# Kernel optimization log

Hardware: AMD Instinct MI355X
Metric: run time of the kernel (lower is better)

The kernel has to match this reference:

```python
import jax, jax.numpy as jnp
import numpy as np

B, N, FEAT, BB, LD = 512, 50, 300, 300, 2048
D1 = BB + FEAT        # 600 = s_with_bb dim
D2 = 2 * D1           # 1200 = combined dim


def _fc(x, w, b):
    # ReLUWithWeightNormFC: weight-norm is a reparametrization of a plain
    # linear, so math-equivalently ReLU(x @ W^T + b).
    return jax.nn.relu(x @ w.T + b)


def setup_inputs() -> dict:
    key = jax.random.key(0)
    ks = jax.random.split(key, 32)

    def p(k, shape):
        return jax.random.normal(k, shape, dtype=jnp.float32) * 0.02

    inp = {
        "l": jax.random.normal(ks[0], (B, LD), dtype=jnp.float32),
        "s": jax.random.normal(ks[1], (B, N, FEAT), dtype=jnp.float32),
        "ps": jax.random.uniform(ks[2], (B, N, 4), dtype=jnp.float32),
        "mask_s": jax.random.randint(ks[3], (B,), 0, 50, dtype=jnp.int32),
        "bb_w": p(ks[4], (BB, 10)),       "bb_b": p(ks[5], (BB,)),
        "fa1_w": p(ks[6], (D1, D1)),      "fa1_b": p(ks[7], (D1,)),
        "fa2_w": p(ks[8], (D1, D1)),      "fa2_b": p(ks[9], (D1,)),
        "fa3_w": p(ks[10], (D2, D2)),     "fa3_b": p(ks[11], (D2,)),
        "fa4_w": p(ks[12], (D2, D2)),     "fa4_b": p(ks[13], (D2,)),
        "fa5_w": p(ks[14], (D2, D2)),     "fa5_b": p(ks[15], (D2,)),
        "lp1_w": p(ks[16], (D2, LD)),     "lp1_b": p(ks[17], (D2,)),
        "lp2_w": p(ks[18], (D2, LD)),     "lp2_b": p(ks[19], (D2,)),
        "out_w": p(ks[20], (FEAT, D2)),   "out_b": p(ks[21], (FEAT,)),
    }
    return inp


def reference(l, s, ps, mask_s,
              bb_w, bb_b, fa1_w, fa1_b, fa2_w, fa2_b, fa3_w, fa3_b,
              fa4_w, fa4_b, fa5_w, fa5_b, lp1_w, lp1_b, lp2_w, lp2_b,
              out_w, out_b):
    # ---- bb_process ----
    size = ps[..., 2:] - ps[..., :2]                       # [B,N,2]
    centre = ps[..., :2] + 0.5 * size                      # [B,N,2]
    area = (size[..., 0] * size[..., 1])[..., None]        # [B,N,1]
    shape = (size[..., 0] / (size[..., 1] + 1e-14))[..., None]
    bb_in = jnp.concatenate([ps, size, centre, area, shape], axis=-1)  # [B,N,10]
    bb = _fc(bb_in, bb_w, bb_b)                            # [B,N,BB]

    s_bb = jnp.concatenate([s, bb], axis=-1)               # [B,N,D1]

    # ---- masked adjacency bias (order of assignments preserved) ----
    i = jnp.arange(N)
    mx = jnp.maximum(i[None, :], i[:, None])               # [N,N]
    m1 = mx[None, :, :] < mask_s[:, None, None]            # [B,N,N]
    m2 = i[None, :, None] >= mask_s[:, None, None]         # row index >= mask_s
    inf_tmp = jnp.where(m1 | m2, 0.0, -jnp.inf)
    inf_tmp = jnp.where(jnp.eye(N, dtype=bool)[None], -jnp.inf, inf_tmp)
    inf_tmp = inf_tmp.at[:, 0, 0].set(
        jnp.where(mask_s == 1, 0.0, inf_tmp[:, 0, 0]))

    # l projections are identical across the 50 nodes -> compute once, broadcast
    lp1 = _fc(l, lp1_w, lp1_b)[:, None, :]                 # [B,1,D2]
    lp2 = _fc(l, lp2_w, lp2_b)[:, None, :]                 # [B,1,D2]

    # ---- one GNN iteration (it=1) ----
    combined = jnp.concatenate(
        [s_bb, _fc(s_bb, fa1_w, fa1_b) * _fc(s_bb, fa2_w, fa2_b)], axis=-1)  # [B,N,D2]
    l_masked_source = _fc(combined, fa3_w, fa3_b) * lp1    # [B,N,D2]
    adj = jnp.einsum('bnd,bmd->bnm', _fc(combined, fa4_w, fa4_b),
                     l_masked_source)                      # [B,N,N]
    adj = jax.nn.softmax(adj + inf_tmp, axis=2)
    prepared = _fc(combined, fa5_w, fa5_b) * lp2           # [B,N,D2]
    messages = _fc(jnp.einsum('bnm,bmd->bnd', adj, prepared), out_w, out_b)
    s_out = jnp.concatenate([s, messages], axis=-1)        # [B,N,2*FEAT]

    output_mask = (i[None, :] < mask_s[:, None])[:, :, None]  # [B,N,1]
    return s_out * output_mask.astype(s_out.dtype), adj
```

## Files before the change

kernel.cpp:

```cpp
#include <hip/hip_runtime.h>
#include <stdint.h>

typedef unsigned short u16;
typedef unsigned int u32;
typedef __attribute__((ext_vector_type(8))) __bf16 bf16x8;
typedef __attribute__((ext_vector_type(4))) float f32x4;

#define DEVINL static __device__ __forceinline__

DEVINL u16 f2bf(float x) {
  u32 u = __float_as_uint(x);
  return (u16)((u + (((u >> 16) & 1u) + 0x7fffu)) >> 16);
}
DEVINL float bf2f(u16 h) { return __uint_as_float(((u32)h) << 16); }

DEVINL void async16(const void* g, void* l) {
  void* g2 = const_cast<void*>(g);
  __builtin_amdgcn_global_load_lds((__attribute__((address_space(1))) void*)g2,
                                   (__attribute__((address_space(3))) void*)l,
                                   16, 0, 0);
}

DEVINL void swz_xy(int& bx, int& by) {
  const int gx = (int)gridDim.x;
  const int nwg = gx * (int)gridDim.y;
  const int bid = (int)blockIdx.y * gx + (int)blockIdx.x;
  const int q = nwg >> 3, r = nwg & 7, x = bid & 7, t = bid >> 3;
  const int s = (x < r ? x * (q + 1) : r * (q + 1) + (x - r) * q) + t;
  bx = s % gx;
  by = s / gx;
}


__global__ void k_pack_w(const float* src, int n, int k, u16* hi, u16* lo,
                         int KP, long total, int gap) {
  long i = (long)blockIdx.x * 256 + threadIdx.x;
  if (i >= total) return;
  int r = (int)(i / KP);
  int c = (int)(i - (long)r * KP);
  int sc = c;
  bool ok = (r < n);
  if (gap) {
    if (c >= 600 && c < 640) ok = false;
    else if (c >= 640) sc = c - 40;
  }
  if (sc >= k) ok = false;
  float x = ok ? src[(size_t)r * k + sc] : 0.f;
  u16 h = f2bf(x);
  hi[i] = h;
  if (lo) lo[i] = f2bf(x - bf2f(h));
}

__global__ void k_pack_bias(const float* src, int n, float* dst, int NP) {
  int i = blockIdx.x * 256 + threadIdx.x;
  if (i < NP) dst[i] = (i < n) ? src[i] : 0.f;
}

__global__ void k_bb(const float* s_c, const float* ps_c, const float* bb_w,
                     const float* bb_b, u16* Chi, u16* Clo) {
  int rn = blockIdx.x;
  const float* p = ps_c + (size_t)rn * 4;
  float p0 = p[0], p1 = p[1], p2 = p[2], p3 = p[3];
  float sz0 = p2 - p0, sz1 = p3 - p1;
  float bin[10];
  bin[0] = p0; bin[1] = p1; bin[2] = p2; bin[3] = p3;
  bin[4] = sz0; bin[5] = sz1;
  bin[6] = p0 + 0.5f * sz0; bin[7] = p1 + 0.5f * sz1;
  bin[8] = sz0 * sz1; bin[9] = sz0 / (sz1 + 1e-14f);
  for (int c = threadIdx.x; c < 640; c += 256) {
    float x = 0.f;
    if (c < 300) {
      x = s_c[(size_t)rn * 300 + c];
    } else if (c < 600) {
      int j = c - 300;
      float a = bb_b[j];
      const float* wr = bb_w + j * 10;
#pragma unroll
      for (int kk = 0; kk < 10; ++kk) a += bin[kk] * wr[kk];
      x = fmaxf(a, 0.f);
    }
    u16 h = f2bf(x);
    Chi[(size_t)rn * 1280 + c] = h;
    Clo[(size_t)rn * 1280 + c] = f2bf(x - bf2f(h));
  }
}


DEVINL void gemm_fused3(const u16* Ahp, const u16* Alp, const u16* Bhp,
                        const u16* Blp, int lda, int ldw, int ksteps,
                        u16* S, f32x4 (&acc)[4][4]) {
  const int tid = threadIdx.x;
  const int lane = tid & 63;
  const int wv = tid >> 6;
  const int wr = (wv >> 1) * 64;
  const int wc = (wv & 1) * 64;
  const int mrow = lane & 15;
  const int q = lane >> 4;

  const int c0 = tid, c1 = tid + 256;
  const int p0 = ((c0 & 3) ^ ((c0 >> 3) & 3)) * 8;
  const int p1 = ((c1 & 3) ^ ((c1 >> 3) & 3)) * 8;
  const long ao0 = (long)(c0 >> 2) * lda + p0;
  const long ao1 = (long)(c1 >> 2) * lda + p1;
  const long bo0 = (long)(c0 >> 2) * ldw + p0;
  const long bo1 = (long)(c1 >> 2) * ldw + p1;

  int aoffs[4], boffs[4];
#pragma unroll
  for (int k = 0; k < 4; ++k) {
    const int ra = wr + mrow + 16 * k;
    const int rb = wc + mrow + 16 * k;
    aoffs[k] = ra * 32 + ((q ^ ((ra >> 1) & 3)) << 3);
    boffs[k] = rb * 32 + ((q ^ ((rb >> 1) & 3)) << 3);
  }

  auto issue = [&](int sl, int t) {
    const long ta = (long)t * 32;
    u16* d = S + sl * 16384;
    async16(Ahp + ta + ao0, d + c0 * 8);
    async16(Ahp + ta + ao1, d + c1 * 8);
    async16(Alp + ta + ao0, d + 4096 + c0 * 8);
    async16(Alp + ta + ao1, d + 4096 + c1 * 8);
    async16(Bhp + ta + bo0, d + 8192 + c0 * 8);
    async16(Bhp + ta + bo1, d + 8192 + c1 * 8);
    async16(Blp + ta + bo0, d + 12288 + c0 * 8);
    async16(Blp + ta + bo1, d + 12288 + c1 * 8);
  };

  issue(0, 0);
  for (int i = 0; i < ksteps; ++i) {
    asm volatile("s_waitcnt vmcnt(0)" ::: "memory");
    __builtin_amdgcn_sched_barrier(0);
    __builtin_amdgcn_s_barrier();
    __builtin_amdgcn_sched_barrier(0);
    if (i + 1 < ksteps) issue((i + 1) & 1, i + 1);
    const u16* Sb = S + (i & 1) * 16384;
    bf16x8 ah[4], al[4], bh[4], bl[4];
#pragma unroll
    for (int k = 0; k < 4; ++k) {
      ah[k] = *(const bf16x8*)(Sb + aoffs[k]);
      al[k] = *(const bf16x8*)(Sb + 4096 + aoffs[k]);
      bh[k] = *(const bf16x8*)(Sb + 8192 + boffs[k]);
      bl[k] = *(const bf16x8*)(Sb + 12288 + boffs[k]);
    }
#pragma unroll
    for (int mi = 0; mi < 4; ++mi)
#pragma unroll
      for (int nj = 0; nj < 4; ++nj)
        acc[mi][nj] = __builtin_amdgcn_mfma_f32_16x16x32_bf16(
            ah[mi], bh[nj], acc[mi][nj], 0, 0, 0);
#pragma unroll
    for (int mi = 0; mi < 4; ++mi)
#pragma unroll
      for (int nj = 0; nj < 4; ++nj)
        acc[mi][nj] = __builtin_amdgcn_mfma_f32_16x16x32_bf16(
            al[mi], bh[nj], acc[mi][nj], 0, 0, 0);
#pragma unroll
    for (int mi = 0; mi < 4; ++mi)
#pragma unroll
      for (int nj = 0; nj < 4; ++nj)
        acc[mi][nj] = __builtin_amdgcn_mfma_f32_16x16x32_bf16(
            ah[mi], bl[nj], acc[mi][nj], 0, 0, 0);
  }
}

DEVINL void gemm_core1(const u16* Ab, const u16* Bb, int lda, int ldw,
                       int ksteps, u16* As, u16* Bs, f32x4 (&acc)[4][4]) {
  const int tid = threadIdx.x;
  const int lane = tid & 63;
  const int wv = tid >> 6;
  const int wr = (wv >> 1) * 64;
  const int wc = (wv & 1) * 64;
  const int mrow = lane & 15;
  const int q = lane >> 4;

  const int c0 = tid, c1 = tid + 256;
  const int p0 = ((c0 & 3) ^ ((c0 >> 3) & 3)) * 8;
  const int p1 = ((c1 & 3) ^ ((c1 >> 3) & 3)) * 8;
  const long ao0 = (long)(c0 >> 2) * lda + p0;
  const long ao1 = (long)(c1 >> 2) * lda + p1;
  const long bo0 = (long)(c0 >> 2) * ldw + p0;
  const long bo1 = (long)(c1 >> 2) * ldw + p1;

  int aoffs[4], boffs[4];
#pragma unroll
  for (int k = 0; k < 4; ++k) {
    const int ra = wr + mrow + 16 * k;
    const int rb = wc + mrow + 16 * k;
    aoffs[k] = ra * 32 + ((q ^ ((ra >> 1) & 3)) << 3);
    boffs[k] = rb * 32 + ((q ^ ((rb >> 1) & 3)) << 3);
  }

  auto issue = [&](int sl, int t) {
    const long ta = (long)t * 32;
    u16* dA = As + sl * 4096;
    u16* dB = Bs + sl * 4096;
    async16(Ab + ta + ao0, dA + c0 * 8);
    async16(Ab + ta + ao1, dA + c1 * 8);
    async16(Bb + ta + bo0, dB + c0 * 8);
    async16(Bb + ta + bo1, dB + c1 * 8);
  };

  issue(0, 0);
  if (ksteps > 1) issue(1, 1);
  if (ksteps > 2) issue(2, 2);
  for (int i = 0; i < ksteps; ++i) {
    if (i + 2 < ksteps)      asm volatile("s_waitcnt vmcnt(8)" ::: "memory");
    else if (i + 1 < ksteps) asm volatile("s_waitcnt vmcnt(4)" ::: "memory");
    else                     asm volatile("s_waitcnt vmcnt(0)" ::: "memory");
    __builtin_amdgcn_sched_barrier(0);
    __builtin_amdgcn_s_barrier();
    __builtin_amdgcn_sched_barrier(0);
    if (i + 3 < ksteps) issue((i + 3) & 3, i + 3);
    const u16* Sa = As + (i & 3) * 4096;
    const u16* Sb = Bs + (i & 3) * 4096;
    bf16x8 af[4], bv[4];
#pragma unroll
    for (int k = 0; k < 4; ++k) af[k] = *(const bf16x8*)(Sa + aoffs[k]);
#pragma unroll
    for (int k = 0; k < 4; ++k) bv[k] = *(const bf16x8*)(Sb + boffs[k]);
#pragma unroll
    for (int mi = 0; mi < 4; ++mi)
#pragma unroll
      for (int nj = 0; nj < 4; ++nj)
        acc[mi][nj] = __builtin_amdgcn_mfma_f32_16x16x32_bf16(
            af[mi], bv[nj], acc[mi][nj], 0, 0, 0);
  }
}

DEVINL void gemm_core2(const u16* const Aph[3], const u16* const B1ph[3],
                       const u16* const B2ph[3], int lda, int ldw, int ksteps,
                       u16* As, u16* B1s, u16* B2s, f32x4 (&a1)[4][4],
                       f32x4 (&a2)[4][4]) {
  const int tid = threadIdx.x;
  const int lane = tid & 63;
  const int wv = tid >> 6;
  const int wr = (wv >> 1) * 64;
  const int wc = (wv & 1) * 64;
  const int mrow = lane & 15;
  const int q = lane >> 4;

  const int c0 = tid, c1 = tid + 256;
  const int p0 = ((c0 & 3) ^ ((c0 >> 3) & 3)) * 8;
  const int p1 = ((c1 & 3) ^ ((c1 >> 3) & 3)) * 8;
  const long ao0 = (long)(c0 >> 2) * lda + p0;
  const long ao1 = (long)(c1 >> 2) * lda + p1;
  const long bo0 = (long)(c0 >> 2) * ldw + p0;
  const long bo1 = (long)(c1 >> 2) * ldw + p1;

  int aoffs[4], boffs[4];
#pragma unroll
  for (int k = 0; k < 4; ++k) {
    const int ra = wr + mrow + 16 * k;
    const int rb = wc + mrow + 16 * k;
    aoffs[k] = ra * 32 + ((q ^ ((ra >> 1) & 3)) << 3);
    boffs[k] = rb * 32 + ((q ^ ((rb >> 1) & 3)) << 3);
  }

  const u16* Aa1 = Aph[1]; const u16* Ba1 = B1ph[1]; const u16* Ca1 = B2ph[1];
  const u16* Aa2 = Aph[2]; const u16* Ba2 = B1ph[2]; const u16* Ca2 = B2ph[2];
  const u16* An = Aph[0];  const u16* Bn = B1ph[0];  const u16* Cn = B2ph[0];
  int tn = 0, pn = 0;
  const int total = 3 * ksteps;

  auto issue = [&](int sl) {
    const u16* ga = An + (long)tn * 32;
    const u16* g1 = Bn + (long)tn * 32;
    const u16* g2 = Cn + (long)tn * 32;
    u16* dA = As + sl * 4096;
    u16* d1 = B1s + sl * 4096;
    u16* d2 = B2s + sl * 4096;
    async16(ga + ao0, dA + c0 * 8);
    async16(ga + ao1, dA + c1 * 8);
    async16(g1 + bo0, d1 + c0 * 8);
    async16(g1 + bo1, d1 + c1 * 8);
    async16(g2 + bo0, d2 + c0 * 8);
    async16(g2 + bo1, d2 + c1 * 8);
    if (++tn == ksteps) {
      tn = 0; ++pn;
      if (pn == 1) { An = Aa1; Bn = Ba1; Cn = Ca1; }
      else if (pn == 2) { An = Aa2; Bn = Ba2; Cn = Ca2; }
    }
  };

  issue(0);
  issue(1);
  int slot = 0;
  for (int i = 0; i < total; ++i) {
    if (i + 1 < total) asm volatile("s_waitcnt vmcnt(6)" ::: "memory");
    else               asm volatile("s_waitcnt vmcnt(0)" ::: "memory");
    __builtin_amdgcn_sched_barrier(0);
    __builtin_amdgcn_s_barrier();
    __builtin_amdgcn_sched_barrier(0);
    if (i + 2 < total) {
      int s2 = slot + 2; if (s2 >= 3) s2 -= 3;
      issue(s2);
    }
    const u16* Sa = As + slot * 4096;
    const u16* S1 = B1s + slot * 4096;
    const u16* S2 = B2s + slot * 4096;
    bf16x8 af[4], b1v[4], b2v[4];
#pragma unroll
    for (int k = 0; k < 4; ++k) af[k] = *(const bf16x8*)(Sa + aoffs[k]);
#pragma unroll
    for (int k = 0; k < 4; ++k) b1v[k] = *(const bf16x8*)(S1 + boffs[k]);
#pragma unroll
    for (int k = 0; k < 4; ++k) b2v[k] = *(const bf16x8*)(S2 + boffs[k]);
#pragma unroll
    for (int mi = 0; mi < 4; ++mi)
#pragma unroll
      for (int nj = 0; nj < 4; ++nj)
        a1[mi][nj] = __builtin_amdgcn_mfma_f32_16x16x32_bf16(
            af[mi], b1v[nj], a1[mi][nj], 0, 0, 0);
#pragma unroll
    for (int mi = 0; mi < 4; ++mi)
#pragma unroll
      for (int nj = 0; nj < 4; ++nj)
        a2[mi][nj] = __builtin_amdgcn_mfma_f32_16x16x32_bf16(
            af[mi], b2v[nj], a2[mi][nj], 0, 0, 0);
    if (++slot == 3) slot = 0;
  }
}

#define GEMM_EPI_IDX                                                    \
  const int lane = threadIdx.x & 63, wv = threadIdx.x >> 6;             \
  const int wr = (wv >> 1) * 64, wc = (wv & 1) * 64;                    \
  const int mcol = lane & 15, q = lane >> 4;                            \
  const int gm0 = by * 128, gn0 = bx * 128;

__global__ __launch_bounds__(256) void k_gemm_fa12(const u16* Ah, const u16* Al,
    const u16* W1h, const u16* W1l, const u16* W2h, const u16* W2l,
    const float* bias, u16* Chi, u16* Clo) {
  __shared__ __align__(16) u16 As[12288], B1s[12288], B2s[12288];
  int bx, by; swz_xy(bx, by);
  const size_t arow = (size_t)by * 128 * 1280;
  const size_t wrow = (size_t)bx * 128 * 640;
  const u16* Aph[3]  = {Ah + arow, Al + arow, Ah + arow};
  const u16* B1ph[3] = {W1h + wrow, W1h + wrow, W1l + wrow};
  const u16* B2ph[3] = {W2h + wrow, W2h + wrow, W2l + wrow};
  f32x4 a1[4][4] = {}, a2[4][4] = {};
  gemm_core2(Aph, B1ph, B2ph, 1280, 640, 20, As, B1s, B2s, a1, a2);
  GEMM_EPI_IDX
#pragma unroll
  for (int mi = 0; mi < 4; ++mi)
#pragma unroll
    for (int r = 0; r < 4; ++r) {
      int grow = gm0 + wr + mi * 16 + q * 4 + r;
#pragma unroll
      for (int ni = 0; ni < 4; ++ni) {
        int gcol = gn0 + wc + ni * 16 + mcol;
        float v1 = fmaxf(a1[mi][ni][r] + bias[gcol], 0.f);
        float v2 = fmaxf(a2[mi][ni][r] + bias[640 + gcol], 0.f);
        float y = v1 * v2;
        u16 h = f2bf(y);
        Chi[(size_t)grow * 1280 + 640 + gcol] = h;
        Clo[(size_t)grow * 1280 + 640 + gcol] = f2bf(y - bf2f(h));
      }
    }
}

__global__ __launch_bounds__(256) void k_gemm_lp(const u16* Ah, const u16* Al,
    const u16* Wh, const u16* Wl, const float* bias, float* outp) {
  __shared__ __align__(16) u16 S[32768];
  int bx, by; swz_xy(bx, by);
  const size_t arow = (size_t)by * 128 * 2048;
  const size_t wrow = (size_t)bx * 128 * 2048;
  f32x4 acc[4][4] = {};
  gemm_fused3(Ah + arow, Al + arow, Wh + wrow, Wl + wrow, 2048, 2048, 64, S,
              acc);
  GEMM_EPI_IDX
#pragma unroll
  for (int mi = 0; mi < 4; ++mi)
#pragma unroll
    for (int r = 0; r < 4; ++r) {
      int grow = gm0 + wr + mi * 16 + q * 4 + r;
#pragma unroll
      for (int ni = 0; ni < 4; ++ni) {
        int gcol = gn0 + wc + ni * 16 + mcol;
        outp[(size_t)grow * 2560 + gcol] = fmaxf(acc[mi][ni][r] + bias[gcol], 0.f);
      }
    }
}

__global__ __launch_bounds__(256) void k_gemm_fa345(const u16* Ah, const u16* Al,
    const u16* Wh, const u16* Wl, const u16* W5h, const float* b34,
    const float* b5, const float* lp_o, u16* fa3h, u16* fa3l, u16* fa4h,
    u16* fa4l, u16* fa5o, int r0) {
  __shared__ __align__(16) u16 S[32768];
  int bx, by; swz_xy(bx, by);
  const size_t arow = (size_t)by * 128 * 1280;
  const int gn0 = bx * 128;
  f32x4 acc[4][4] = {};
  if (gn0 < 2560) {
    const size_t wrow = (size_t)gn0 * 1280;
    gemm_fused3(Ah + arow, Al + arow, Wh + wrow, Wl + wrow, 1280, 1280, 40, S,
                acc);
  } else {
    const size_t wrow = (size_t)(gn0 - 2560) * 1280;
    gemm_core1(Ah + arow, W5h + wrow, 1280, 1280, 40, S, S + 16384, acc);
  }
  const int lane = threadIdx.x & 63, wv = threadIdx.x >> 6;
  const int wr = (wv >> 1) * 64, wc = (wv & 1) * 64;
  const int mcol = lane & 15, q = lane >> 4;
  const int gm0 = by * 128;
  if (gn0 < 2560) {
    const int seg = (gn0 >= 1280);
    u16* dsth = seg ? fa4h : fa3h;
    u16* dstl = seg ? fa4l : fa3l;
#pragma unroll
    for (int mi = 0; mi < 4; ++mi)
#pragma unroll
      for (int r = 0; r < 4; ++r) {
        int grow = gm0 + wr + mi * 16 + q * 4 + r;
        int b = (r0 + grow) / 50;
        const float* lpb = lp_o + (size_t)b * 2560;
#pragma unroll
        for (int ni = 0; ni < 4; ++ni) {
          int gcol = gn0 + wc + ni * 16 + mcol;
          int c = seg ? gcol - 1280 : gcol;
          float v = fmaxf(acc[mi][ni][r] + b34[gcol], 0.f);
          if (!seg) v *= lpb[c];
          if (c < 1216) {
            u16 h = f2bf(v);
            dsth[(size_t)grow * 1216 + c] = h;
            dstl[(size_t)grow * 1216 + c] = f2bf(v - bf2f(h));
          }
        }
      }
  } else {
#pragma unroll
    for (int mi = 0; mi < 4; ++mi)
#pragma unroll
      for (int r = 0; r < 4; ++r) {
        int grow = gm0 + wr + mi * 16 + q * 4 + r;
        int b = (r0 + grow) / 50;
        const float* lpb = lp_o + (size_t)b * 2560 + 1280;
#pragma unroll
        for (int ni = 0; ni < 4; ++ni) {
          int gcol = (gn0 - 2560) + wc + ni * 16 + mcol;
          float v = fmaxf(acc[mi][ni][r] + b5[gcol], 0.f) * lpb[gcol];
          if (gcol < 1216) fa5o[(size_t)grow * 1216 + gcol] = f2bf(v);
        }
      }
  }
}

__global__ __launch_bounds__(256) void k_gemm_out(const u16* A, const u16* Wh,
    const float* bias, const int* mask_s, float* outp, int r0) {
  __shared__ __align__(16) u16 S[32768];
  int bx, by; swz_xy(bx, by);
  const size_t arow = (size_t)by * 128 * 1216;
  const size_t wrow = (size_t)bx * 128 * 1216;
  f32x4 acc[4][4] = {};
  gemm_core1(A + arow, Wh + wrow, 1216, 1216, 38, S, S + 16384, acc);
  GEMM_EPI_IDX
#pragma unroll
  for (int mi = 0; mi < 4; ++mi)
#pragma unroll
    for (int r = 0; r < 4; ++r) {
      int grow = r0 + gm0 + wr + mi * 16 + q * 4 + r;
      int b = grow / 50;
      int n = grow - b * 50;
      float keep = (n < mask_s[b]) ? 1.f : 0.f;
#pragma unroll
      for (int ni = 0; ni < 4; ++ni) {
        int gcol = gn0 + wc + ni * 16 + mcol;
        float v = fmaxf(acc[mi][ni][r] + bias[gcol], 0.f) * keep;
        if (gcol < 300) outp[(size_t)grow * 600 + 300 + gcol] = v;
      }
    }
}

__global__ __launch_bounds__(256) void k_attn(const u16* fa3h, const u16* fa3l,
    const u16* fa4h, const u16* fa4l, const u16* fa5o, const int* mask_s,
    float* adj_out, u16* msg, int b0) {
  __shared__ __align__(16) u16 stg[4096];
  __shared__ float Ssc[64 * 64];
  const int bl = blockIdx.x;
  const int bg = b0 + bl;
  const int tid = threadIdx.x, lane = tid & 63, wv = tid >> 6;
  const int mrow = lane & 15, q = lane >> 4;
  const size_t base = (size_t)bl * 50 * 1216;

  {
    const int srow = tid >> 2;
    const int srcRow = srow < 50 ? srow : 49;
    const size_t gsoff = base + (size_t)srcRow * 1216 + (tid & 3) * 8;
    u16* lA = stg + tid * 8;
    u16* lB = stg + 2048 + tid * 8;
    f32x4 acc[4] = {};
    for (int p = 0; p < 3; ++p) {
      const u16* Ap = (p == 1) ? fa4l : fa4h;
      const u16* Bp = (p == 2) ? fa3l : fa3h;
      for (int t = 0; t < 38; ++t) {
        __syncthreads();
        async16(Ap + gsoff + t * 32, lA);
        async16(Bp + gsoff + t * 32, lB);
        __syncthreads();
        bf16x8 af = *(const bf16x8*)(stg + (wv * 16 + mrow) * 32 + q * 8);
#pragma unroll
        for (int ni = 0; ni < 4; ++ni) {
          bf16x8 bv = *(const bf16x8*)(stg + 2048 + (ni * 16 + mrow) * 32 + q * 8);
          acc[ni] =
              __builtin_amdgcn_mfma_f32_16x16x32_bf16(af, bv, acc[ni], 0, 0, 0);
        }
      }
    }
#pragma unroll
    for (int ni = 0; ni < 4; ++ni)
#pragma unroll
      for (int r = 0; r < 4; ++r)
        Ssc[(wv * 16 + q * 4 + r) * 64 + ni * 16 + mrow] = acc[ni][r];
  }
  __syncthreads();

  {
    const int mk = mask_s[bg];
    for (int n = wv; n < 50; n += 4) {
      int mm = lane;
      float v = -__builtin_inff();
      if (mm < 50) {
        int mx2 = n > mm ? n : mm;
        bool valid = (mx2 < mk) || (n >= mk);
        if (mm == n) valid = false;
        if (n == 0 && mm == 0 && mk == 1) valid = true;
        if (valid) v = Ssc[n * 64 + mm];
      }
      float mx = v;
      for (int o = 32; o > 0; o >>= 1) mx = fmaxf(mx, __shfl_down(mx, o));
      mx = __shfl(mx, 0);
      float e = __expf(v - mx);
      float sm = e;
      for (int o = 32; o > 0; o >>= 1) sm += __shfl_down(sm, o);
      sm = __shfl(sm, 0);
      float pv = e / sm;
      if (mm < 50) {
        adj_out[((size_t)bg * 50 + n) * 50 + mm] = pv;
        Ssc[n * 64 + mm] = pv;
      } else {
        Ssc[n * 64 + mm] = 0.f;
      }
    }
  }
  __syncthreads();

  {
    const int c0 = tid, c1 = tid + 256;
    const int m0 = c0 >> 3, d0 = (c0 & 7) * 8;
    const int m1 = c1 >> 3, d1 = (c1 & 7) * 8;
    const size_t g0 = base + (size_t)(m0 < 50 ? m0 : 49) * 1216 + d0;
    const size_t g1 = base + (size_t)(m1 < 50 ? m1 : 49) * 1216 + d1;
    for (int dt = 0; dt < 19; ++dt) {
      __syncthreads();
      async16(fa5o + g0 + dt * 64, stg + c0 * 8);
      async16(fa5o + g1 + dt * 64, stg + c1 * 8);
      __syncthreads();
      f32x4 a3[4] = {};
#pragma unroll
      for (int ks = 0; ks < 2; ++ks) {
        bf16x8 af;
#pragma unroll
        for (int j = 0; j < 8; ++j)
          af[j] = (__bf16)Ssc[(wv * 16 + mrow) * 64 + ks * 32 + q * 8 + j];
#pragma unroll
        for (int ni = 0; ni < 4; ++ni) {
          bf16x8 bv;
#pragma unroll
          for (int j = 0; j < 8; ++j)
            bv[j] = *(const __bf16*)(stg + (ks * 32 + q * 8 + j) * 64 + ni * 16 + mrow);
          a3[ni] = __builtin_amdgcn_mfma_f32_16x16x32_bf16(af, bv, a3[ni], 0, 0, 0);
        }
      }
#pragma unroll
      for (int ni = 0; ni < 4; ++ni)
#pragma unroll
        for (int r = 0; r < 4; ++r) {
          int n = wv * 16 + q * 4 + r;
          if (n < 50)
            msg[((size_t)bl * 50 + n) * 1216 + dt * 64 + ni * 16 + mrow] =
                f2bf(a3[ni][r]);
        }
    }
  }
}

__global__ void k_write_s(const float* s, const int* mask_s, float* outp) {
  long i = (long)blockIdx.x * 256 + threadIdx.x;
  if (i >= 7680000L) return;
  int rn = (int)(i / 300);
  int c = (int)(i - (long)rn * 300);
  int b = rn / 50;
  int n = rn - b * 50;
  outp[(size_t)rn * 600 + c] = (n < mask_s[b]) ? s[i] : 0.f;
}

extern "C" void kernel_launch(void* const* d_in, const int* in_sizes, int n_in,
                              void* d_out_, int out_size, void* d_ws,
                              size_t ws_size, hipStream_t stream) {
  (void)in_sizes; (void)n_in; (void)out_size;
  const float* l_in = (const float*)d_in[0];
  const float* s_in = (const float*)d_in[1];
  const float* ps   = (const float*)d_in[2];
  const int*   msk  = (const int*)d_in[3];
  const float* bbw  = (const float*)d_in[4];
  const float* bbb  = (const float*)d_in[5];
  const float* fa1w = (const float*)d_in[6];
  const float* fa1b = (const float*)d_in[7];
  const float* fa2w = (const float*)d_in[8];
  const float* fa2b = (const float*)d_in[9];
  const float* fa3w = (const float*)d_in[10];
  const float* fa3b = (const float*)d_in[11];
  const float* fa4w = (const float*)d_in[12];
  const float* fa4b = (const float*)d_in[13];
  const float* fa5w = (const float*)d_in[14];
  const float* fa5b = (const float*)d_in[15];
  const float* lp1w = (const float*)d_in[16];
  const float* lp1b = (const float*)d_in[17];
  const float* lp2w = (const float*)d_in[18];
  const float* lp2b = (const float*)d_in[19];
  const float* outw = (const float*)d_in[20];
  const float* outb = (const float*)d_in[21];
  float* outp = (float*)d_out_;

  char* wsb = (char*)d_ws;
  size_t off = 0;
  auto alloc = [&](size_t bytes) -> char* {
    char* p = wsb + off;
    off = (off + bytes + 255) & ~(size_t)255;
    return p;
  };
  u16*   l_hi   = (u16*)alloc(512ull * 2048 * 2);
  u16*   l_lo   = (u16*)alloc(512ull * 2048 * 2);
  u16*   Wout   = (u16*)alloc(384ull * 1216 * 2);
  float* b_fa12 = (float*)alloc(1280 * 4);
  float* b_fa34 = (float*)alloc(2560 * 4);
  float* b_fa5  = (float*)alloc(1280 * 4);
  float* b_lp   = (float*)alloc(2560 * 4);
  float* b_out  = (float*)alloc(384 * 4);
  float* lp_o   = (float*)alloc(512ull * 2560 * 4);
  u16*   slab   = (u16*)alloc(10485760ull * 2);
  u16* Wlph   = slab;
  u16* Wlpl   = slab + 5242880;
  u16* Wfa1h  = slab;
  u16* Wfa1l  = slab + 409600;
  u16* Wfa2h  = slab + 819200;
  u16* Wfa2l  = slab + 1228800;
  u16* Wfa34h = slab + 1638400;
  u16* Wfa34l = slab + 4915200;
  u16* Wfa5h  = slab + 8192000;

  size_t ws_eff = ws_size ? ws_size : (size_t)512 * 1024 * 1024;
  long RN = 3200;
  const long opts[4] = {25600, 12800, 6400, 3200};
  for (int i = 0; i < 4; ++i) {
    size_t need = off + (size_t)17280 * opts[i] + 8 * 256;
    if (need <= ws_eff) { RN = opts[i]; break; }
  }
  u16*  Chi  = (u16*)alloc((size_t)RN * 1280 * 2);
  u16*  Clo  = (u16*)alloc((size_t)RN * 1280 * 2);
  u16*  fa5o = (u16*)alloc((size_t)RN * 1216 * 2);
  u16*  fa3h = (u16*)alloc((size_t)RN * 1216 * 2);
  u16*  fa3l = (u16*)alloc((size_t)RN * 1216 * 2);
  u16*  fa4h = (u16*)alloc((size_t)RN * 1216 * 2);
  u16*  fa4l = (u16*)alloc((size_t)RN * 1216 * 2);
  u16*  msg  = Chi;
  float* adj_o = outp + 15360000;

  dim3 T(256);
  k_pack_bias<<<dim3(3), T, 0, stream>>>(fa1b, 600, b_fa12, 640);
  k_pack_bias<<<dim3(3), T, 0, stream>>>(fa2b, 600, b_fa12 + 640, 640);
  k_pack_bias<<<dim3(5), T, 0, stream>>>(fa3b, 1200, b_fa34, 1280);
  k_pack_bias<<<dim3(5), T, 0, stream>>>(fa4b, 1200, b_fa34 + 1280, 1280);
  k_pack_bias<<<dim3(5), T, 0, stream>>>(fa5b, 1200, b_fa5, 1280);
  k_pack_bias<<<dim3(5), T, 0, stream>>>(lp1b, 1200, b_lp, 1280);
  k_pack_bias<<<dim3(5), T, 0, stream>>>(lp2b, 1200, b_lp + 1280, 1280);
  k_pack_bias<<<dim3(2), T, 0, stream>>>(outb, 300, b_out, 384);

  auto packw = [&](const float* src, int n, int k, u16* hi, u16* lo, int KP,
                   long total, int gap) {
    k_pack_w<<<dim3((unsigned)((total + 255) / 256)), T, 0, stream>>>(
        src, n, k, hi, lo, KP, total, gap);
  };
  packw(l_in, 512, 2048, l_hi, l_lo, 2048, 512L * 2048, 0);
  packw(outw, 300, 1200, Wout, nullptr, 1216, 384L * 1216, 0);

  packw(lp1w, 1200, 2048, Wlph, Wlpl, 2048, 1280L * 2048, 0);
  packw(lp2w, 1200, 2048, Wlph + 1280 * 2048, Wlpl + 1280 * 2048, 2048,
        1280L * 2048, 0);
  k_gemm_lp<<<dim3(20, 4), T, 0, stream>>>(l_hi, l_lo, Wlph, Wlpl, b_lp, lp_o);

  packw(fa1w, 600, 600, Wfa1h, Wfa1l, 640, 640L * 640, 0);
  packw(fa2w, 600, 600, Wfa2h, Wfa2l, 640, 640L * 640, 0);
  packw(fa3w, 1200, 1200, Wfa34h, Wfa34l, 1280, 1280L * 1280, 1);
  packw(fa4w, 1200, 1200, Wfa34h + 1638400, Wfa34l + 1638400, 1280,
        1280L * 1280, 1);
  packw(fa5w, 1200, 1200, Wfa5h, nullptr, 1280, 1280L * 1280, 1);

  const int nch = (int)(25600 / RN);
  const unsigned gy = (unsigned)(RN / 128);
  for (int c = 0; c < nch; ++c) {
    const int r0 = (int)(c * RN);
    const int b0 = r0 / 50;
    k_bb<<<dim3((unsigned)RN), T, 0, stream>>>(s_in + (size_t)r0 * 300,
                                               ps + (size_t)r0 * 4, bbw, bbb,
                                               Chi, Clo);
    k_gemm_fa12<<<dim3(5, gy), T, 0, stream>>>(Chi, Clo, Wfa1h, Wfa1l, Wfa2h,
                                               Wfa2l, b_fa12, Chi, Clo);
    k_gemm_fa345<<<dim3(30, gy), T, 0, stream>>>(Chi, Clo, Wfa34h, Wfa34l,
                                                 Wfa5h, b_fa34, b_fa5, lp_o,
                                                 fa3h, fa3l, fa4h, fa4l, fa5o,
                                                 r0);
    k_attn<<<dim3((unsigned)(RN / 50)), T, 0, stream>>>(fa3h, fa3l, fa4h, fa4l,
                                                        fa5o, msk, adj_o, msg,
                                                        b0);
    k_gemm_out<<<dim3(3, gy), T, 0, stream>>>(msg, Wout, b_out, msk, outp, r0);
  }
  k_write_s<<<dim3(30000), T, 0, stream>>>(s_in, msk, outp);
}
```

Before: 1.499 ms.

## Deepen async LDS pipelines in GEMMs and attention, fuse masked s copy into k_bb

Every GEMM core now keeps more k-tiles in flight. The fused hi/lo GEMM goes from double to triple buffering, the single-precision core from 4 to 6 stages, and the attention kernel's score and message loops get 8-slot async prefetch rings in place of sync-load-sync per tile. The attention A-tile loads now use swizzled LDS offsets to reduce bank conflicts. The separate masked copy of s into the output is folded into k_bb, which removes a whole launch and a re-read of s. The deeper pipelines raise LDS use per block (96KB GEMM, larger attention staging), which can lower occupancy.

```diff
diff --git a/kernel.cpp b/kernel.cpp
--- a/kernel.cpp
+++ b/kernel.cpp
@@ -57,8 +57,13 @@
 }
 
 __global__ void k_bb(const float* s_c, const float* ps_c, const float* bb_w,
-                     const float* bb_b, u16* Chi, u16* Clo) {
+                     const float* bb_b, const int* mask_s, u16* Chi, u16* Clo,
+                     float* outp, int r0) {
   int rn = blockIdx.x;
+  int grow = r0 + rn;
+  int b = grow / 50;
+  int n = grow - b * 50;
+  float keep = (n < mask_s[b]) ? 1.f : 0.f;
   const float* p = ps_c + (size_t)rn * 4;
   float p0 = p[0], p1 = p[1], p2 = p[2], p3 = p[3];
   float sz0 = p2 - p0, sz1 = p3 - p1;
@@ -71,6 +76,7 @@
     float x = 0.f;
     if (c < 300) {
       x = s_c[(size_t)rn * 300 + c];
+      outp[(size_t)grow * 600 + c] = keep * x;
     } else if (c < 600) {
       int j = c - 300;
       float a = bb_b[j];
@@ -128,13 +134,17 @@
   };
 
   issue(0, 0);
+  if (ksteps > 1) issue(1, 1);
+  int cs = 0, is = 2;
   for (int i = 0; i < ksteps; ++i) {
-    asm volatile("s_waitcnt vmcnt(0)" ::: "memory");
+    if (i + 1 < ksteps) asm volatile("s_waitcnt vmcnt(8)" ::: "memory");
+    else                asm volatile("s_waitcnt vmcnt(0)" ::: "memory");
     __builtin_amdgcn_sched_barrier(0);
     __builtin_amdgcn_s_barrier();
     __builtin_amdgcn_sched_barrier(0);
-    if (i + 1 < ksteps) issue((i + 1) & 1, i + 1);
-    const u16* Sb = S + (i & 1) * 16384;
+    if (i + 2 < ksteps) { issue(is, i + 2); if (++is == 3) is = 0; }
+    const u16* Sb = S + cs * 16384;
+    if (++cs == 3) cs = 0;
     bf16x8 ah[4], al[4], bh[4], bl[4];
 #pragma unroll
     for (int k = 0; k < 4; ++k) {
@@ -201,19 +211,23 @@
     async16(Bb + ta + bo1, dB + c1 * 8);
   };
 
-  issue(0, 0);
-  if (ksteps > 1) issue(1, 1);
-  if (ksteps > 2) issue(2, 2);
+  const int npro = ksteps < 5 ? ksteps : 5;
+  for (int j = 0; j < npro; ++j) issue(j, j);
+  int cs = 0, is = 5;
   for (int i = 0; i < ksteps; ++i) {
-    if (i + 2 < ksteps)      asm volatile("s_waitcnt vmcnt(8)" ::: "memory");
-    else if (i + 1 < ksteps) asm volatile("s_waitcnt vmcnt(4)" ::: "memory");
-    else                     asm volatile("s_waitcnt vmcnt(0)" ::: "memory");
+    const int rem = ksteps - 1 - i;
+    if (rem >= 4)      asm volatile("s_waitcnt vmcnt(16)" ::: "memory");
+    else if (rem == 3) asm volatile("s_waitcnt vmcnt(12)" ::: "memory");
+    else if (rem == 2) asm volatile("s_waitcnt vmcnt(8)" ::: "memory");
+    else if (rem == 1) asm volatile("s_waitcnt vmcnt(4)" ::: "memory");
+    else               asm volatile("s_waitcnt vmcnt(0)" ::: "memory");
     __builtin_amdgcn_sched_barrier(0);
     __builtin_amdgcn_s_barrier();
     __builtin_amdgcn_sched_barrier(0);
-    if (i + 3 < ksteps) issue((i + 3) & 3, i + 3);
-    const u16* Sa = As + (i & 3) * 4096;
-    const u16* Sb = Bs + (i & 3) * 4096;
+    if (i + 5 < ksteps) { issue(is, i + 5); if (++is == 6) is = 0; }
+    const u16* Sa = As + cs * 4096;
+    const u16* Sb = Bs + cs * 4096;
+    if (++cs == 6) cs = 0;
     bf16x8 af[4], bv[4];
 #pragma unroll
     for (int k = 0; k < 4; ++k) af[k] = *(const bf16x8*)(Sa + aoffs[k]);
@@ -361,7 +375,7 @@
 
 __global__ __launch_bounds__(256) void k_gemm_lp(const u16* Ah, const u16* Al,
     const u16* Wh, const u16* Wl, const float* bias, float* outp) {
-  __shared__ __align__(16) u16 S[32768];
+  __shared__ __align__(16) u16 S[49152];
   int bx, by; swz_xy(bx, by);
   const size_t arow = (size_t)by * 128 * 2048;
   const size_t wrow = (size_t)bx * 128 * 2048;
@@ -386,7 +400,7 @@
     const u16* Wh, const u16* Wl, const u16* W5h, const float* b34,
     const float* b5, const float* lp_o, u16* fa3h, u16* fa3l, u16* fa4h,
     u16* fa4l, u16* fa5o, int r0) {
-  __shared__ __align__(16) u16 S[32768];
+  __shared__ __align__(16) u16 S[49152];
   int bx, by; swz_xy(bx, by);
   const size_t arow = (size_t)by * 128 * 1280;
   const int gn0 = bx * 128;
@@ -397,7 +411,7 @@
                 acc);
   } else {
     const size_t wrow = (size_t)(gn0 - 2560) * 1280;
-    gemm_core1(Ah + arow, W5h + wrow, 1280, 1280, 40, S, S + 16384, acc);
+    gemm_core1(Ah + arow, W5h + wrow, 1280, 1280, 40, S, S + 24576, acc);
   }
   const int lane = threadIdx.x & 63, wv = threadIdx.x >> 6;
   const int wr = (wv >> 1) * 64, wc = (wv & 1) * 64;
@@ -447,12 +461,12 @@
 
 __global__ __launch_bounds__(256) void k_gemm_out(const u16* A, const u16* Wh,
     const float* bias, const int* mask_s, float* outp, int r0) {
-  __shared__ __align__(16) u16 S[32768];
+  __shared__ __align__(16) u16 S[49152];
   int bx, by; swz_xy(bx, by);
   const size_t arow = (size_t)by * 128 * 1216;
   const size_t wrow = (size_t)bx * 128 * 1216;
   f32x4 acc[4][4] = {};
-  gemm_core1(A + arow, Wh + wrow, 1216, 1216, 38, S, S + 16384, acc);
+  gemm_core1(A + arow, Wh + wrow, 1216, 1216, 38, S, S + 24576, acc);
   GEMM_EPI_IDX
 #pragma unroll
   for (int mi = 0; mi < 4; ++mi)
@@ -474,7 +488,7 @@
 __global__ __launch_bounds__(256) void k_attn(const u16* fa3h, const u16* fa3l,
     const u16* fa4h, const u16* fa4l, const u16* fa5o, const int* mask_s,
     float* adj_out, u16* msg, int b0) {
-  __shared__ __align__(16) u16 stg[4096];
+  __shared__ __align__(16) u16 stg[32768];
   __shared__ float Ssc[64 * 64];
   const int bl = blockIdx.x;
   const int bg = b0 + bl;
@@ -485,25 +499,49 @@
   {
     const int srow = tid >> 2;
     const int srcRow = srow < 50 ? srow : 49;
-    const size_t gsoff = base + (size_t)srcRow * 1216 + (tid & 3) * 8;
-    u16* lA = stg + tid * 8;
-    u16* lB = stg + 2048 + tid * 8;
-    f32x4 acc[4] = {};
-    for (int p = 0; p < 3; ++p) {
+    const size_t gsoff = base + (size_t)srcRow * 1216 +
+                         (size_t)(((tid & 3) ^ ((tid >> 3) & 3)) * 8);
+    auto issueP1 = [&](int sl, int s) {
+      const int p = (s >= 76) ? 2 : (s >= 38 ? 1 : 0);
+      const int t = s - p * 38;
       const u16* Ap = (p == 1) ? fa4l : fa4h;
       const u16* Bp = (p == 2) ? fa3l : fa3h;
-      for (int t = 0; t < 38; ++t) {
-        __syncthreads();
-        async16(Ap + gsoff + t * 32, lA);
-        async16(Bp + gsoff + t * 32, lB);
-        __syncthreads();
-        bf16x8 af = *(const bf16x8*)(stg + (wv * 16 + mrow) * 32 + q * 8);
-#pragma unroll
-        for (int ni = 0; ni < 4; ++ni) {
-          bf16x8 bv = *(const bf16x8*)(stg + 2048 + (ni * 16 + mrow) * 32 + q * 8);
-          acc[ni] =
-              __builtin_amdgcn_mfma_f32_16x16x32_bf16(af, bv, acc[ni], 0, 0, 0);
-        }
+      u16* d = stg + sl * 4096;
+      async16(Ap + gsoff + (size_t)t * 32, d + tid * 8);
+      async16(Bp + gsoff + (size_t)t * 32, d + 2048 + tid * 8);
+    };
+    const int ra = wv * 16 + mrow;
+    const int aoff = ra * 32 + ((q ^ ((ra >> 1) & 3)) << 3);
+    int boff[4];
+#pragma unroll
+    for (int ni = 0; ni < 4; ++ni) {
+      const int rb = ni * 16 + mrow;
+      boff[ni] = rb * 32 + ((q ^ ((rb >> 1) & 3)) << 3);
+    }
+    for (int j = 0; j < 7; ++j) issueP1(j, j);
+    f32x4 acc[4] = {};
+    int cs = 0, is = 7;
+    for (int i = 0; i < 114; ++i) {
+      const int rem = 113 - i;
+      if (rem >= 6)      asm volatile("s_waitcnt vmcnt(12)" ::: "memory");
+      else if (rem == 5) asm volatile("s_waitcnt vmcnt(10)" ::: "memory");
+      else if (rem == 4) asm volatile("s_waitcnt vmcnt(8)" ::: "memory");
+      else if (rem == 3) asm volatile("s_waitcnt vmcnt(6)" ::: "memory");
+      else if (rem == 2) asm volatile("s_waitcnt vmcnt(4)" ::: "memory");
+      else if (rem == 1) asm volatile("s_waitcnt vmcnt(2)" ::: "memory");
+      else               asm volatile("s_waitcnt vmcnt(0)" ::: "memory");
+      __builtin_amdgcn_sched_barrier(0);
+      __builtin_amdgcn_s_barrier();
+      __builtin_amdgcn_sched_barrier(0);
+      if (i + 7 < 114) { issueP1(is, i + 7); if (++is == 8) is = 0; }
+      const u16* d = stg + cs * 4096;
+      if (++cs == 8) cs = 0;
+      bf16x8 af = *(const bf16x8*)(d + aoff);
+#pragma unroll
+      for (int ni = 0; ni < 4; ++ni) {
+        bf16x8 bv = *(const bf16x8*)(d + 2048 + boff[ni]);
+        acc[ni] =
+            __builtin_amdgcn_mfma_f32_16x16x32_bf16(af, bv, acc[ni], 0, 0, 0);
       }
     }
 #pragma unroll
@@ -513,6 +551,18 @@
         Ssc[(wv * 16 + q * 4 + r) * 64 + ni * 16 + mrow] = acc[ni][r];
   }
   __syncthreads();
+
+  const int c0 = tid, c1 = tid + 256;
+  const int m0 = c0 >> 3, d0 = (c0 & 7) * 8;
+  const int m1 = c1 >> 3, d1 = (c1 & 7) * 8;
+  const size_t g0 = base + (size_t)(m0 < 50 ? m0 : 49) * 1216 + d0;
+  const size_t g1 = base + (size_t)(m1 < 50 ? m1 : 49) * 1216 + d1;
+  auto issueP3 = [&](int sl, int s) {
+    u16* d = stg + sl * 4096;
+    async16(fa5o + g0 + (size_t)s * 64, d + c0 * 8);
+    async16(fa5o + g1 + (size_t)s * 64, d + c1 * 8);
+  };
+  for (int j = 0; j < 7; ++j) issueP3(j, j);
 
   {
     const int mk = mask_s[bg];
@@ -545,16 +595,22 @@
   __syncthreads();
 
   {
-    const int c0 = tid, c1 = tid + 256;
-    const int m0 = c0 >> 3, d0 = (c0 & 7) * 8;
-    const int m1 = c1 >> 3, d1 = (c1 & 7) * 8;
-    const size_t g0 = base + (size_t)(m0 < 50 ? m0 : 49) * 1216 + d0;
-    const size_t g1 = base + (size_t)(m1 < 50 ? m1 : 49) * 1216 + d1;
+    int cs = 0, is = 7;
     for (int dt = 0; dt < 19; ++dt) {
-      __syncthreads();
-      async16(fa5o + g0 + dt * 64, stg + c0 * 8);
-      async16(fa5o + g1 + dt * 64, stg + c1 * 8);
-      __syncthreads();
+      const int rem = 18 - dt;
+      if (rem >= 6)      asm volatile("s_waitcnt vmcnt(12)" ::: "memory");
+      else if (rem == 5) asm volatile("s_waitcnt vmcnt(10)" ::: "memory");
+      else if (rem == 4) asm volatile("s_waitcnt vmcnt(8)" ::: "memory");
+      else if (rem == 3) asm volatile("s_waitcnt vmcnt(6)" ::: "memory");
+      else if (rem == 2) asm volatile("s_waitcnt vmcnt(4)" ::: "memory");
+      else if (rem == 1) asm volatile("s_waitcnt vmcnt(2)" ::: "memory");
+      else               asm volatile("s_waitcnt vmcnt(0)" ::: "memory");
+      __builtin_amdgcn_sched_barrier(0);
+      __builtin_amdgcn_s_barrier();
+      __builtin_amdgcn_sched_barrier(0);
+      if (dt + 7 < 19) { issueP3(is, dt + 7); if (++is == 8) is = 0; }
+      const u16* d = stg + cs * 4096;
+      if (++cs == 8) cs = 0;
       f32x4 a3[4] = {};
 #pragma unroll
       for (int ks = 0; ks < 2; ++ks) {
@@ -567,7 +623,7 @@
           bf16x8 bv;
 #pragma unroll
           for (int j = 0; j < 8; ++j)
-            bv[j] = *(const __bf16*)(stg + (ks * 32 + q * 8 + j) * 64 + ni * 16 + mrow);
+            bv[j] = *(const __bf16*)(d + (ks * 32 + q * 8 + j) * 64 + ni * 16 + mrow);
           a3[ni] = __builtin_amdgcn_mfma_f32_16x16x32_bf16(af, bv, a3[ni], 0, 0, 0);
         }
       }
@@ -582,16 +638,6 @@
         }
     }
   }
-}
-
-__global__ void k_write_s(const float* s, const int* mask_s, float* outp) {
-  long i = (long)blockIdx.x * 256 + threadIdx.x;
-  if (i >= 7680000L) return;
-  int rn = (int)(i / 300);
-  int c = (int)(i - (long)rn * 300);
-  int b = rn / 50;
-  int n = rn - b * 50;
-  outp[(size_t)rn * 600 + c] = (n < mask_s[b]) ? s[i] : 0.f;
 }
 
 extern "C" void kernel_launch(void* const* d_in, const int* in_sizes, int n_in,
@@ -703,7 +749,7 @@
     const int b0 = r0 / 50;
     k_bb<<<dim3((unsigned)RN), T, 0, stream>>>(s_in + (size_t)r0 * 300,
                                                ps + (size_t)r0 * 4, bbw, bbb,
-                                               Chi, Clo);
+                                               msk, Chi, Clo, outp, r0);
     k_gemm_fa12<<<dim3(5, gy), T, 0, stream>>>(Chi, Clo, Wfa1h, Wfa1l, Wfa2h,
                                                Wfa2l, b_fa12, Chi, Clo);
     k_gemm_fa345<<<dim3(30, gy), T, 0, stream>>>(Chi, Clo, Wfa34h, Wfa34l,
@@ -715,5 +761,4 @@
                                                         b0);
     k_gemm_out<<<dim3(3, gy), T, 0, stream>>>(msg, Wout, b_out, msk, outp, r0);
   }
-  k_write_s<<<dim3(30000), T, 0, stream>>>(s_in, msk, outp);
-}
+}
```

Measured after the change: 1.745 ms. +16.4%, slower.
